# Performance work log

Hardware: AMD Instinct MI355X
Metric: run time of the kernel (lower is better)

Reference implementation:

```python
import jax, jax.numpy as jnp
import numpy as np
from jax import lax

N, IC, OC, K, SDIM, H, W = 16, 512, 512, 3, 512, 32, 32
PAD, STRIDE, LR = 1, 1, 1.0
WEIGHT_SCALER = 1.0 / np.sqrt(IC * K * K) * LR   # equalized-lr conv scale
FC_SCALER = 1.0 / np.sqrt(SDIM) * LR             # equalized-lr fc scale


def setup_inputs() -> dict:
    key = jax.random.key(0)
    k1, k2, k3 = jax.random.split(key, 3)
    x = jax.random.normal(k1, (N, IC, H, W), dtype=jnp.float32)
    style = jax.random.normal(k2, (N, SDIM), dtype=jnp.float32)
    weight = jax.random.normal(k3, (OC, IC, K, K), dtype=jnp.float32)  # std = 1/lr = 1
    fc_weight = jax.random.normal(jax.random.fold_in(key, 10), (IC, SDIM), dtype=jnp.float32)
    fc_bias = jnp.zeros((IC,), dtype=jnp.float32)
    return {"x": x, "style": style, "weight": weight,
            "fc_weight": fc_weight, "fc_bias": fc_bias}


def reference(x, style, weight, fc_weight, fc_bias):
    # EqualizedFullyConnect + AddChannelwiseBias, then +1 -> modulation rates [N, iC]
    mod = jnp.einsum('ns,cs->nc', style, fc_weight) * FC_SCALER + fc_bias * LR + 1.0
    # modulated per-sample weight [N, oC, iC, kH, kW]
    w = WEIGHT_SCALER * weight[None] * mod[:, None, :, None, None]
    # demodulate: rsqrt of sum of squares over (iC, kH, kW)
    demod = lax.rsqrt(jnp.sum(w * w, axis=(2, 3, 4)) + 1e-8)  # [N, oC]
    w = w * demod[:, :, None, None, None]
    # grouped conv with groups=N == per-sample conv: vmap over batch
    def conv1(xi, wi):
        # xi: [iC,H,W], wi: [oC,iC,kH,kW]
        return lax.conv_general_dilated(
            xi[None], wi, window_strides=(STRIDE, STRIDE),
            padding=((PAD, PAD), (PAD, PAD)),
            dimension_numbers=('NCHW', 'OIHW', 'NCHW'))[0]
    out = jax.vmap(conv1)(x, w)  # [N, oC, H, W]
    return out
```

## Files before the change

### kernel.cpp

```cpp
#include <hip/hip_runtime.h>
#include <hip/hip_bf16.h>

#define N_    16
#define IC_   512
#define OC_   512
#define SDIM_ 512
#define H_    32
#define W_    32
#define HW_   1024

#define FC_SCALER 0.04419417382415922f
#define WS_       0.014731391274719738f
#define WS2_      (1.0f/4608.0f)

typedef __attribute__((__ext_vector_type__(8)))  __bf16 bf16x8;
typedef __attribute__((__ext_vector_type__(16))) float  f32x16;
typedef __attribute__((__ext_vector_type__(4)))  int    i32x4;

typedef __attribute__((address_space(1))) const unsigned int GInt;
typedef __attribute__((address_space(3))) unsigned int LInt;

#define WAIT0()  asm volatile("s_waitcnt vmcnt(0)"  ::: "memory")
#define WAIT3()  asm volatile("s_waitcnt vmcnt(3)"  ::: "memory")

__device__ __forceinline__ unsigned short f2bf(float f) {
    unsigned int u = __builtin_bit_cast(unsigned int, f);
    unsigned int r = (u + 0x7FFFu + ((u >> 16) & 1u)) >> 16;
    return (unsigned short)r;
}

__global__ void k_mod(const float* __restrict__ style, const float* __restrict__ fcw,
                      const float* __restrict__ fcb, float* __restrict__ mod) {
    int gid = blockIdx.x * blockDim.x + threadIdx.x;
    int wid = gid >> 6, lane = gid & 63;
    if (wid >= N_ * IC_) return;
    int n = wid >> 9, c = wid & 511;
    const float4* sp = (const float4*)(style + n * SDIM_);
    const float4* wp = (const float4*)(fcw + (size_t)c * SDIM_);
    float acc = 0.f;
    for (int i = lane; i < SDIM_ / 4; i += 64) {
        float4 a = sp[i], b = wp[i];
        acc += a.x*b.x + a.y*b.y + a.z*b.z + a.w*b.w;
    }
#pragma unroll
    for (int off = 32; off; off >>= 1) acc += __shfl_xor(acc, off);
    if (lane == 0) mod[wid] = acc * FC_SCALER + fcb[c] + 1.0f;
}

__global__ void k_wprep(const float* __restrict__ w, unsigned short* __restrict__ wt,
                        float* __restrict__ wsq) {
    int tid = blockIdx.x * blockDim.x + threadIdx.x;
    int oc = tid >> 9, ic = tid & 511;
    int og = oc >> 7, ocl = oc & 127;
    int icc = ic >> 5, ks = (ic >> 3) & 3, i8 = ic & 7;
    float s = 0.f;
#pragma unroll
    for (int t = 0; t < 9; t++) {
        float v = w[(size_t)tid * 9 + t];
        s += v * v;
        size_t off = ((((size_t)t * 4 + og) * 16 + icc) * 4 + ks) * 1024
                   + (size_t)ocl * 8 + i8;
        wt[off] = f2bf(v);
    }
    wsq[tid] = s;
}

__global__ void k_demod(const float* __restrict__ mod, const float* __restrict__ wsq,
                        float* __restrict__ demod_ws) {
    int gid = blockIdx.x * blockDim.x + threadIdx.x;
    int wid = gid >> 6, lane = gid & 63;
    if (wid >= N_ * OC_) return;
    int n = wid >> 9, oc = wid & 511;
    const float4* mp = (const float4*)(mod + n * IC_);
    const float4* qp = (const float4*)(wsq + (size_t)oc * IC_);
    float acc = 0.f;
    for (int i = lane; i < IC_ / 4; i += 64) {
        float4 m = mp[i], q = qp[i];
        acc += m.x*m.x*q.x + m.y*m.y*q.y + m.z*m.z*q.z + m.w*m.w*q.w;
    }
#pragma unroll
    for (int off = 32; off; off >>= 1) acc += __shfl_xor(acc, off);
    if (lane == 0) {
        float s = WS2_ * acc + 1e-8f;
        demod_ws[wid] = WS_ / sqrtf(s);
    }
}

__global__ void k_premod(const float* __restrict__ x, const float* __restrict__ mod,
                         unsigned short* __restrict__ xm) {
    __shared__ __align__(16) unsigned short t_lds[64][80];
    int bx = blockIdx.x;
    int n = bx >> 7, hwt = (bx >> 3) & 15, ict = bx & 7;
    int hw0 = hwt * 64, ic0 = ict * 64;
    int tid = threadIdx.x, lane = tid & 63, ty = tid >> 6;
#pragma unroll
    for (int jj = 0; jj < 16; jj++) {
        int icl = ty * 16 + jj;
        float v = x[(size_t)(n * IC_ + ic0 + icl) * HW_ + hw0 + lane]
                  * mod[n * IC_ + ic0 + icl];
        t_lds[lane][icl] = f2bf(v);
    }
    __syncthreads();
    int xcol = tid & 31, ks64 = tid >> 5;
    int icc = ict * 2 + (ks64 >> 2), ks = ks64 & 3;
#pragma unroll
    for (int rep = 0; rep < 2; rep++) {
        int hwl = rep * 32 + xcol;
        i32x4 v = *(const i32x4*)&t_lds[hwl][ks64 * 8];
        int y = (hw0 >> 5) + rep;
        size_t off = ((((size_t)n * 16 + icc) * 32 + y) * 4 + ks) * 256 + xcol * 8;
        *(i32x4*)(xm + off) = v;
    }
}

__global__ __launch_bounds__(512, 2)
void k_conv(const unsigned short* __restrict__ xm, const unsigned short* __restrict__ wt,
            const float* __restrict__ demod_ws, float* __restrict__ out) {
    __shared__ __align__(16) char smem[40960 + 49152 + 1024 + 32 + 512];
    unsigned short* xt0   = (unsigned short*)(smem);
    unsigned short* wb0   = (unsigned short*)(smem + 40960);
    unsigned short* trash = (unsigned short*)(smem + 90112);
    float*          zslot = (float*)(smem + 91136);
    float*          s_demod = (float*)(smem + 91168);

    int bx = blockIdx.x;
    int x8 = bx & 7;
    int octg = x8 >> 1;
    int r    = ((bx >> 3) << 1) | (x8 & 1);
    int n = r >> 2, spt = r & 3;
    int oc0 = octg * 128, y0 = spt * 8;

    int tid = threadIdx.x, lane = tid & 63, wid = tid >> 6;
    int l31 = lane & 31, lhi = lane >> 5;
    int wr = wid & 1, wc = (wid >> 1) & 1, kh = wid >> 2;

    if (tid < 128) s_demod[tid] = demod_ws[n * OC_ + oc0 + tid];
    __builtin_amdgcn_sched_barrier(0);

    if (tid == 0) { i32x4 z = {}; *(i32x4*)zslot = z; }
    if (spt == 0 && tid < 128) {
        i32x4 z = {};
        *(i32x4*)&xt0[tid * 8] = z;
        *(i32x4*)&xt0[10240 + tid * 8] = z;
    }
    if (spt == 3 && tid < 128) {
        i32x4 z = {};
        *(i32x4*)&xt0[9 * 1024 + tid * 8] = z;
        *(i32x4*)&xt0[10240 + 9 * 1024 + tid * 8] = z;
    }

    const unsigned short* xsrc_n = xm + (size_t)n * (16 * 32 * 1024);

    auto stage_x = [&](int buf, int icc) {
#pragma unroll
        for (int k = 0; k < 3; k++) {
            int c = wid + k * 8;
            int rr = c >> 1, hh = c & 1;
            int y = y0 - 1 + rr;
            bool oob = (c >= 20) | ((unsigned)y >= 32u) | (icc >= 16);
            int yc = y < 0 ? 0 : (y > 31 ? 31 : y);
            int iccc = icc & 15;
            const unsigned short* g =
                xsrc_n + ((size_t)iccc * 32 + yc) * 1024 + hh * 512 + lane * 8;
            unsigned short* l = oob ? trash
                                    : xt0 + buf * 10240 + rr * 1024 + hh * 512;
            __builtin_amdgcn_global_load_lds((GInt*)g, (LInt*)l, 16, 0, 0);
        }
    };
    auto stage_w = [&](int set, int p, int icc) {
#pragma unroll
        for (int k = 0; k < 3; k++) {
            int tap = k * 3 + p;
            const unsigned short* g =
                wt + ((((size_t)tap * 4 + octg) * 16 + icc) * 4096) + wid * 512 + lane * 8;
            unsigned short* l = wb0 + set * 12288 + k * 4096 + wid * 512;
            __builtin_amdgcn_global_load_lds((GInt*)g, (LInt*)l, 16, 0, 0);
        }
    };

    f32x16 acc[2][4] = {};

    stage_x(0, 0);
    stage_w(0, 0, 0);
    asm volatile("s_waitcnt lgkmcnt(0)" ::: "memory");

    int xb = 0;
    int kso = kh * 2 + lhi;
#pragma unroll 1
    for (int icc = 0; icc < 16; icc++) {
#pragma unroll 1
        for (int p = 0; p < 3; p++) {
            if (p == 1) WAIT3(); else WAIT0();
            __builtin_amdgcn_s_barrier();
            int g1 = icc * 3 + p + 1;
            if (g1 < 48) stage_w(g1 & 1, g1 % 3, g1 / 3);
            if (p == 0) stage_x(xb ^ 1, icc + 1);

            const unsigned short* xtb = xt0 + xb * 10240;
            const unsigned short* wbp = wb0 + ((icc * 3 + p) & 1) * 12288;
            int col = l31 + p - 1;
            bool oobc = (unsigned)col >= 32u;
            bf16x8 r6[6];
#pragma unroll
            for (int j = 0; j < 6; j++) {
                int rr = wc * 4 + j;
                const unsigned short* src = oobc ? (const unsigned short*)zslot
                    : xtb + rr * 1024 + kso * 256 + col * 8;
                r6[j] = *(const bf16x8*)src;
            }
#pragma unroll
            for (int dy = 0; dy < 3; dy++) {
                bf16x8 af0 = *(const bf16x8*)(wbp + dy * 4096 + kso * 1024
                                              + (wr * 64 + l31) * 8);
                bf16x8 af1 = *(const bf16x8*)(wbp + dy * 4096 + kso * 1024
                                              + (wr * 64 + 32 + l31) * 8);
                __builtin_amdgcn_s_setprio(1);
#pragma unroll
                for (int fs = 0; fs < 4; fs++)
                    acc[0][fs] = __builtin_amdgcn_mfma_f32_32x32x16_bf16(
                        af0, r6[fs + dy], acc[0][fs], 0, 0, 0);
#pragma unroll
                for (int fs = 0; fs < 4; fs++)
                    acc[1][fs] = __builtin_amdgcn_mfma_f32_32x32x16_bf16(
                        af1, r6[fs + dy], acc[1][fs], 0, 0, 0);
                __builtin_amdgcn_s_setprio(0);
            }
        }
        xb ^= 1;
    }

    __syncthreads();
    float* exch = (float*)smem;
#pragma unroll
    for (int fo = 0; fo < 2; fo++) {
        if (kh) {
#pragma unroll
            for (int fs = 0; fs < 4; fs++)
#pragma unroll
                for (int rg = 0; rg < 16; rg++)
                    exch[(((wid & 3) * 4 + fs) * 16 + rg) * 64 + lane] = acc[fo][fs][rg];
        }
        __syncthreads();
        if (!kh) {
#pragma unroll
            for (int fs = 0; fs < 4; fs++) {
                int y = y0 + wc * 4 + fs;
#pragma unroll
                for (int rg = 0; rg < 16; rg++) {
                    int row = (rg & 3) + 8 * (rg >> 2) + 4 * lhi;
                    int ocl = wr * 64 + fo * 32 + row;
                    float v = acc[fo][fs][rg]
                            + exch[((wid * 4 + fs) * 16 + rg) * 64 + lane];
                    v *= s_demod[ocl];
                    out[((size_t)(n * OC_ + oc0 + ocl) * H_ + y) * W_ + l31] = v;
                }
            }
        }
        __syncthreads();
    }
}

extern "C" void kernel_launch(void* const* d_in, const int* in_sizes, int n_in,
                              void* d_out, int out_size, void* d_ws, size_t ws_size,
                              hipStream_t stream) {
    const float* x      = (const float*)d_in[0];
    const float* style  = (const float*)d_in[1];
    const float* weight = (const float*)d_in[2];
    const float* fcw    = (const float*)d_in[3];
    const float* fcb    = (const float*)d_in[4];
    float* out = (float*)d_out;

    char* ws = (char*)d_ws;
    float*          mod   = (float*)ws;
    float*          demod = (float*)(ws + 32768);
    float*          wsq   = (float*)(ws + 65536);
    unsigned short* wtb   = (unsigned short*)(ws + 65536 + 1048576);
    unsigned short* xmb   = (unsigned short*)(ws + 65536 + 1048576 + 4718592);

    k_mod   <<<2048, 256, 0, stream>>>(style, fcw, fcb, mod);
    k_wprep <<<1024, 256, 0, stream>>>(weight, wtb, wsq);
    k_demod <<<2048, 256, 0, stream>>>(mod, wsq, demod);
    k_premod<<<2048, 256, 0, stream>>>(x, mod, xmb);
    k_conv  <<<256,  512, 0, stream>>>(xmb, wtb, demod, out);
}
```

Baseline: 98.50 us.

## Halve conv block OC tile to 64, double grid, triple-buffer weight staging

The conv kernel now uses 256-thread blocks covering 64 output channels instead of 512-thread blocks covering 128, so the grid doubles to 512 blocks. The weight layout in the prep kernel is changed to match. Weight staging moves from double to triple buffering with a two-step prefetch distance, and the wait counts are adjusted. The blockIdx mapping is reordered to group batch samples, and the epilogue reduction is done in a single exchange pass. The aim is better CU occupancy on 256 CUs and more latency hiding for weight loads. In exchange, each block reuses the x tile over fewer output channels, which raises x traffic.

```diff
diff --git a/kernel.cpp b/kernel.cpp
--- a/kernel.cpp
+++ b/kernel.cpp
@@ -20,8 +20,9 @@
 typedef __attribute__((address_space(1))) const unsigned int GInt;
 typedef __attribute__((address_space(3))) unsigned int LInt;
 
+#define WAIT3()  asm volatile("s_waitcnt vmcnt(3)"  ::: "memory")
+#define WAIT8()  asm volatile("s_waitcnt vmcnt(8)"  ::: "memory")
 #define WAIT0()  asm volatile("s_waitcnt vmcnt(0)"  ::: "memory")
-#define WAIT3()  asm volatile("s_waitcnt vmcnt(3)"  ::: "memory")
 
 __device__ __forceinline__ unsigned short f2bf(float f) {
     unsigned int u = __builtin_bit_cast(unsigned int, f);
@@ -51,15 +52,15 @@
                         float* __restrict__ wsq) {
     int tid = blockIdx.x * blockDim.x + threadIdx.x;
     int oc = tid >> 9, ic = tid & 511;
-    int og = oc >> 7, ocl = oc & 127;
+    int og = oc >> 6, ocl = oc & 63;
     int icc = ic >> 5, ks = (ic >> 3) & 3, i8 = ic & 7;
     float s = 0.f;
 #pragma unroll
     for (int t = 0; t < 9; t++) {
         float v = w[(size_t)tid * 9 + t];
         s += v * v;
-        size_t off = ((((size_t)t * 4 + og) * 16 + icc) * 4 + ks) * 1024
-                   + (size_t)ocl * 8 + i8;
+        size_t off = (((size_t)t * 8 + og) * 16 + icc) * 2048
+                   + (size_t)ks * 512 + ocl * 8 + i8;
         wt[off] = f2bf(v);
     }
     wsq[tid] = s;
@@ -113,28 +114,28 @@
     }
 }
 
-__global__ __launch_bounds__(512, 2)
+__global__ __launch_bounds__(256, 2)
 void k_conv(const unsigned short* __restrict__ xm, const unsigned short* __restrict__ wt,
             const float* __restrict__ demod_ws, float* __restrict__ out) {
-    __shared__ __align__(16) char smem[40960 + 49152 + 1024 + 32 + 512];
-    unsigned short* xt0   = (unsigned short*)(smem);
-    unsigned short* wb0   = (unsigned short*)(smem + 40960);
-    unsigned short* trash = (unsigned short*)(smem + 90112);
-    float*          zslot = (float*)(smem + 91136);
-    float*          s_demod = (float*)(smem + 91168);
+    __shared__ __align__(16) char smem[79136];
+    unsigned short* xt0     = (unsigned short*)(smem);
+    unsigned short* wb0     = (unsigned short*)(smem + 40960);
+    unsigned short* trash   = (unsigned short*)(smem + 77824);
+    float*          zslot   = (float*)(smem + 78848);
+    float*          s_demod = (float*)(smem + 78880);
 
     int bx = blockIdx.x;
-    int x8 = bx & 7;
-    int octg = x8 >> 1;
-    int r    = ((bx >> 3) << 1) | (x8 & 1);
-    int n = r >> 2, spt = r & 3;
-    int oc0 = octg * 128, y0 = spt * 8;
+    int x8 = bx & 7, j = bx >> 3;
+    int n = x8 * 2 + (j >> 5);
+    int rem = j & 31;
+    int octg = rem >> 2, spt = rem & 3;
+    int oc0 = octg * 64, y0 = spt * 8;
 
     int tid = threadIdx.x, lane = tid & 63, wid = tid >> 6;
     int l31 = lane & 31, lhi = lane >> 5;
-    int wr = wid & 1, wc = (wid >> 1) & 1, kh = wid >> 2;
-
-    if (tid < 128) s_demod[tid] = demod_ws[n * OC_ + oc0 + tid];
+    int wc = wid & 1, kh = wid >> 1;
+
+    if (tid < 64) s_demod[tid] = demod_ws[n * OC_ + oc0 + tid];
     __builtin_amdgcn_sched_barrier(0);
 
     if (tid == 0) { i32x4 z = {}; *(i32x4*)zslot = z; }
@@ -153,11 +154,11 @@
 
     auto stage_x = [&](int buf, int icc) {
 #pragma unroll
-        for (int k = 0; k < 3; k++) {
-            int c = wid + k * 8;
+        for (int k = 0; k < 5; k++) {
+            int c = wid + k * 4;
             int rr = c >> 1, hh = c & 1;
             int y = y0 - 1 + rr;
-            bool oob = (c >= 20) | ((unsigned)y >= 32u) | (icc >= 16);
+            bool oob = ((unsigned)y >= 32u) | (icc >= 16);
             int yc = y < 0 ? 0 : (y > 31 ? 31 : y);
             int iccc = icc & 15;
             const unsigned short* g =
@@ -167,13 +168,17 @@
             __builtin_amdgcn_global_load_lds((GInt*)g, (LInt*)l, 16, 0, 0);
         }
     };
-    auto stage_w = [&](int set, int p, int icc) {
+    auto stage_w = [&](int g2) {
+        int gc = g2 < 48 ? g2 : 47;
+        int icc2 = gc / 3, p2 = gc % 3;
+        bool oob = g2 >= 48;
 #pragma unroll
         for (int k = 0; k < 3; k++) {
-            int tap = k * 3 + p;
+            int tap = k * 3 + p2;
             const unsigned short* g =
-                wt + ((((size_t)tap * 4 + octg) * 16 + icc) * 4096) + wid * 512 + lane * 8;
-            unsigned short* l = wb0 + set * 12288 + k * 4096 + wid * 512;
+                wt + (((size_t)tap * 8 + octg) * 16 + icc2) * 2048 + wid * 512 + lane * 8;
+            unsigned short* l = oob ? trash
+                                    : wb0 + (g2 % 3) * 6144 + k * 2048 + wid * 512;
             __builtin_amdgcn_global_load_lds((GInt*)g, (LInt*)l, 16, 0, 0);
         }
     };
@@ -181,7 +186,8 @@
     f32x16 acc[2][4] = {};
 
     stage_x(0, 0);
-    stage_w(0, 0, 0);
+    stage_w(0);
+    stage_w(1);
     asm volatile("s_waitcnt lgkmcnt(0)" ::: "memory");
 
     int xb = 0;
@@ -190,30 +196,28 @@
     for (int icc = 0; icc < 16; icc++) {
 #pragma unroll 1
         for (int p = 0; p < 3; p++) {
-            if (p == 1) WAIT3(); else WAIT0();
+            int g = icc * 3 + p;
+            if (p == 0) WAIT3(); else WAIT8();
             __builtin_amdgcn_s_barrier();
-            int g1 = icc * 3 + p + 1;
-            if (g1 < 48) stage_w(g1 & 1, g1 % 3, g1 / 3);
+            stage_w(g + 2);
             if (p == 0) stage_x(xb ^ 1, icc + 1);
 
             const unsigned short* xtb = xt0 + xb * 10240;
-            const unsigned short* wbp = wb0 + ((icc * 3 + p) & 1) * 12288;
+            const unsigned short* wbp = wb0 + (g % 3) * 6144;
             int col = l31 + p - 1;
             bool oobc = (unsigned)col >= 32u;
             bf16x8 r6[6];
 #pragma unroll
-            for (int j = 0; j < 6; j++) {
-                int rr = wc * 4 + j;
+            for (int jj = 0; jj < 6; jj++) {
+                int rr = wc * 4 + jj;
                 const unsigned short* src = oobc ? (const unsigned short*)zslot
                     : xtb + rr * 1024 + kso * 256 + col * 8;
-                r6[j] = *(const bf16x8*)src;
+                r6[jj] = *(const bf16x8*)src;
             }
 #pragma unroll
             for (int dy = 0; dy < 3; dy++) {
-                bf16x8 af0 = *(const bf16x8*)(wbp + dy * 4096 + kso * 1024
-                                              + (wr * 64 + l31) * 8);
-                bf16x8 af1 = *(const bf16x8*)(wbp + dy * 4096 + kso * 1024
-                                              + (wr * 64 + 32 + l31) * 8);
+                bf16x8 af0 = *(const bf16x8*)(wbp + dy * 2048 + kso * 512 + l31 * 8);
+                bf16x8 af1 = *(const bf16x8*)(wbp + dy * 2048 + kso * 512 + (32 + l31) * 8);
                 __builtin_amdgcn_s_setprio(1);
 #pragma unroll
                 for (int fs = 0; fs < 4; fs++)
@@ -229,34 +233,36 @@
         xb ^= 1;
     }
 
+    WAIT0();
     __syncthreads();
     float* exch = (float*)smem;
-#pragma unroll
-    for (int fo = 0; fo < 2; fo++) {
-        if (kh) {
+    if (kh == 1) {
+#pragma unroll
+        for (int fo = 0; fo < 2; fo++)
 #pragma unroll
             for (int fs = 0; fs < 4; fs++)
 #pragma unroll
                 for (int rg = 0; rg < 16; rg++)
-                    exch[(((wid & 3) * 4 + fs) * 16 + rg) * 64 + lane] = acc[fo][fs][rg];
-        }
-        __syncthreads();
-        if (!kh) {
+                    exch[(((wc * 2 + fo) * 4 + fs) * 16 + rg) * 64 + lane] = acc[fo][fs][rg];
+    }
+    __syncthreads();
+    if (kh == 0) {
+#pragma unroll
+        for (int fo = 0; fo < 2; fo++) {
 #pragma unroll
             for (int fs = 0; fs < 4; fs++) {
                 int y = y0 + wc * 4 + fs;
 #pragma unroll
                 for (int rg = 0; rg < 16; rg++) {
                     int row = (rg & 3) + 8 * (rg >> 2) + 4 * lhi;
-                    int ocl = wr * 64 + fo * 32 + row;
+                    int ocl = fo * 32 + row;
                     float v = acc[fo][fs][rg]
-                            + exch[((wid * 4 + fs) * 16 + rg) * 64 + lane];
+                            + exch[(((wc * 2 + fo) * 4 + fs) * 16 + rg) * 64 + lane];
                     v *= s_demod[ocl];
                     out[((size_t)(n * OC_ + oc0 + ocl) * H_ + y) * W_ + l31] = v;
                 }
             }
         }
-        __syncthreads();
     }
 }
 
@@ -281,5 +287,5 @@
     k_wprep <<<1024, 256, 0, stream>>>(weight, wtb, wsq);
     k_demod <<<2048, 256, 0, stream>>>(mod, wsq, demod);
     k_premod<<<2048, 256, 0, stream>>>(x, mod, xmb);
-    k_conv  <<<256,  512, 0, stream>>>(xmb, wtb, demod, out);
-}
+    k_conv  <<<512,  256, 0, stream>>>(xmb, wtb, demod, out);
+}
```

After: 99.99 us. About the same (+1.5%).
